# Kernel tuning notes

Measured on AMD Instinct MI355X. Metric: run time of the kernel, lower is better.

Reference implementation:

```python
import jax, jax.numpy as jnp
import numpy as np

N, E, IN, H, O, K = 50000, 800000, 256, 128, 32, 5
ALPHA, EPS = 0.1, 1e-5


def setup_inputs() -> dict:
    key = jax.random.key(0)
    ks = jax.random.split(key, 20)
    nrm = lambda k, shape, s=0.02: jax.random.normal(k, shape, dtype=jnp.float32) * s
    H2 = H // 2
    return {
        "x": jax.random.normal(ks[0], (N, IN), dtype=jnp.float32),
        "edge_index": jax.random.randint(ks[1], (2, E), 0, N),
        "edge_weight": jax.random.uniform(ks[2], (E,), dtype=jnp.float32),
        # lin1 + bn1
        "W1": nrm(ks[3], (IN, H)), "b1": jnp.zeros((H,), jnp.float32),
        "g1": jnp.ones((H,), jnp.float32), "be1": jnp.zeros((H,), jnp.float32),
        "m1": nrm(ks[4], (H,), 0.1), "v1": 1.0 + 0.1 * jax.random.uniform(ks[5], (H,), dtype=jnp.float32),
        # lin2 + bn2
        "W2": nrm(ks[6], (H, H)), "b2": jnp.zeros((H,), jnp.float32),
        "g2": jnp.ones((H,), jnp.float32), "be2": jnp.zeros((H,), jnp.float32),
        "m2": nrm(ks[7], (H,), 0.1), "v2": 1.0 + 0.1 * jax.random.uniform(ks[8], (H,), dtype=jnp.float32),
        # attention over hop outputs (K+1)
        "att": jnp.ones((K + 1,), jnp.float32) + nrm(ks[9], (K + 1,), 0.1),
        # head: Linear(H, H//2) + BN + ReLU + Linear(H//2, O)
        "W3": nrm(ks[10], (H, H2)), "b3": jnp.zeros((H2,), jnp.float32),
        "g3": jnp.ones((H2,), jnp.float32), "be3": jnp.zeros((H2,), jnp.float32),
        "m3": nrm(ks[11], (H2,), 0.1), "v3": 1.0 + 0.1 * jax.random.uniform(ks[12], (H2,), dtype=jnp.float32),
        "W4": nrm(ks[13], (H2, O)), "b4": jnp.zeros((O,), jnp.float32),
    }


def _bn(t, g, b, m, v):
    # eval-mode BatchNorm1d using running stats
    return (t - m) * (g / jnp.sqrt(v + EPS)) + b


def reference(x, edge_index, edge_weight, W1, b1, g1, be1, m1, v1,
              W2, b2, g2, be2, m2, v2, att,
              W3, b3, g3, be3, m3, v3, W4, b4):
    n = x.shape[0]
    row, col = edge_index[0], edge_index[1]

    h = jax.nn.relu(_bn(x @ W1 + b1, g1, be1, m1, v1))
    identity = h
    h = jax.nn.relu(_bn(h @ W2 + b2, g2, be2, m2, v2)) + identity

    # weighted edge normalization: out-weight sum per source node, clamped >= 1
    wsum = jnp.maximum(jax.ops.segment_sum(edge_weight, row, num_segments=n), 1.0)
    edge_norm = edge_weight / wsum[row]  # [E]

    def prop(h_in):
        # APPNP-style: K inner iterations blending toward this call's h0
        h0 = h_in
        hk = h_in
        for _ in range(K):
            msg = hk[row] * edge_norm[:, None]          # [E, H] gather + scale
            agg = jax.ops.segment_sum(msg, col, num_segments=n)  # scatter-add
            hk = (1.0 - ALPHA) * agg + ALPHA * h0
        return hk

    xs = [h]
    hc = h
    for _ in range(K):  # outer loop: att has K+1 weights
        hc = prop(hc)
        xs.append(hc)

    stacked = jnp.stack(xs, axis=-1)          # [N, H, K+1]
    w = jax.nn.softmax(att)                   # [K+1]
    fused = jnp.einsum('nhk,k->nh', stacked, w)

    hid = jax.nn.relu(_bn(fused @ W3 + b3, g3, be3, m3, v3))
    return hid @ W4 + b4
```

## Files before the change

kernel.cpp:

```cpp
#include <hip/hip_runtime.h>
#include <cstddef>
#include <cstdint>

namespace {

constexpr int N   = 50000;
constexpr int E   = 800000;
constexpr int IN  = 256;
constexpr int H   = 128;
constexpr int H2v = 64;
constexpr int O   = 32;
constexpr int K   = 5;
constexpr float ALPHA = 0.1f;
constexpr float EPS   = 1e-5f;
constexpr int SCAN_CH = 1024;
constexpr int SCAN_NB = (N + SCAN_CH - 1) / SCAN_CH;

__device__ inline uint32_t pack2_bf16(float x, float y) {
  uint32_t ux = __float_as_uint(x);
  uint32_t uy = __float_as_uint(y);
  ux = (ux + 0x7FFFu + ((ux >> 16) & 1u)) >> 16;
  uy = (uy + 0x7FFFu + ((uy >> 16) & 1u)) & 0xFFFF0000u;
  return uy | ux;
}

__device__ inline float bf16_lo(uint32_t v) { return __uint_as_float(v << 16); }
__device__ inline float bf16_hi(uint32_t v) { return __uint_as_float(v & 0xFFFF0000u); }

__global__ void zero_int_kernel(int* __restrict__ p, int n) {
  int i = blockIdx.x * blockDim.x + threadIdx.x;
  if (i < n) p[i] = 0;
}

__global__ void softmax_att_kernel(const float* __restrict__ att, float* __restrict__ wk) {
  if (threadIdx.x == 0 && blockIdx.x == 0) {
    float mx = att[0];
    for (int i = 1; i < K + 1; ++i) mx = fmaxf(mx, att[i]);
    float ex[K + 1];
    float s = 0.f;
    for (int i = 0; i < K + 1; ++i) { ex[i] = expf(att[i] - mx); s += ex[i]; }
    for (int i = 0; i < K + 1; ++i) wk[i] = ex[i] / s;
  }
}

__global__ void hist_kernel(const int* __restrict__ row, const int* __restrict__ col,
                            const float* __restrict__ ew,
                            int* __restrict__ deg, float* __restrict__ wsum) {
  int i = blockIdx.x * blockDim.x + threadIdx.x;
  if (i < E) {
    atomicAdd(&deg[col[i]], 1);
    atomicAdd(&wsum[row[i]], ew[i]);
  }
}

__global__ __launch_bounds__(256) void scan_local_kernel(const int* __restrict__ deg,
                                                         int* __restrict__ offs,
                                                         int* __restrict__ bsum) {
  __shared__ int sd[256];
  int base = blockIdx.x * SCAN_CH;
  int t = threadIdx.x;
  int v[4];
  int s = 0;
#pragma unroll
  for (int u = 0; u < 4; ++u) {
    int i = base + t * 4 + u;
    v[u] = (i < N) ? deg[i] : 0;
    s += v[u];
  }
  sd[t] = s;
  __syncthreads();
  int val = s;
  for (int off = 1; off < 256; off <<= 1) {
    int x = (t >= off) ? sd[t - off] : 0;
    __syncthreads();
    val += x;
    sd[t] = val;
    __syncthreads();
  }
  int excl = val - s;
#pragma unroll
  for (int u = 0; u < 4; ++u) {
    int i = base + t * 4 + u;
    if (i < N) offs[i] = excl;
    excl += v[u];
  }
  if (t == 255) bsum[blockIdx.x] = val;
}

__global__ void scan_bsum_kernel(int* __restrict__ bsum) {
  if (threadIdx.x == 0 && blockIdx.x == 0) {
    int acc = 0;
    for (int i = 0; i < SCAN_NB; ++i) {
      int v = bsum[i];
      bsum[i] = acc;
      acc += v;
    }
    bsum[SCAN_NB] = acc;
  }
}

__global__ void scan_add_kernel(int* __restrict__ offs, const int* __restrict__ bsum,
                                int* __restrict__ cursor) {
  int i = blockIdx.x * blockDim.x + threadIdx.x;
  if (i < N) {
    int o = offs[i] + bsum[i / SCAN_CH];
    offs[i] = o;
    cursor[i] = o;
  }
  if (i == 0) offs[N] = bsum[SCAN_NB];
}

__global__ void fill_kernel(const int* __restrict__ row, const int* __restrict__ col,
                            const float* __restrict__ ew, const float* __restrict__ wsum,
                            int* __restrict__ cursor, int* __restrict__ csr_src,
                            float* __restrict__ csr_w) {
  int i = blockIdx.x * blockDim.x + threadIdx.x;
  if (i < E) {
    int d = col[i];
    int p = atomicAdd(&cursor[d], 1);
    int s = row[i];
    csr_src[p] = s;
    csr_w[p] = ew[i] / fmaxf(wsum[s], 1.0f);
  }
}

__global__ __launch_bounds__(256) void mlp1_kernel(
    const float* __restrict__ x, const float* __restrict__ W1,
    const float* __restrict__ b1, const float* __restrict__ g1,
    const float* __restrict__ be1, const float* __restrict__ m1,
    const float* __restrict__ v1, float* __restrict__ h1) {
  __shared__ float xl[32][IN];
  int node0 = blockIdx.x * 32;
  int t = threadIdx.x;
  for (int idx = t * 4; idx < 32 * IN; idx += 256 * 4) {
    int r = idx >> 8, c = idx & (IN - 1);
    float4 xv = {0.f, 0.f, 0.f, 0.f};
    if (node0 + r < N) xv = *(const float4*)&x[(size_t)(node0 + r) * IN + c];
    *(float4*)&xl[r][c] = xv;
  }
  __syncthreads();
  int ng = t >> 5;
  int c0 = (t & 31) * 4;
  float acc[4][4];
#pragma unroll
  for (int a = 0; a < 4; ++a)
#pragma unroll
    for (int b = 0; b < 4; ++b) acc[a][b] = 0.f;
  for (int k = 0; k < IN; k += 4) {
    float4 xv[4];
#pragma unroll
    for (int a = 0; a < 4; ++a) xv[a] = *(const float4*)&xl[ng * 4 + a][k];
    float4 wv[4];
#pragma unroll
    for (int j = 0; j < 4; ++j) wv[j] = *(const float4*)&W1[(size_t)(k + j) * H + c0];
#pragma unroll
    for (int a = 0; a < 4; ++a) {
      float xa0 = xv[a].x, xa1 = xv[a].y, xa2 = xv[a].z, xa3 = xv[a].w;
      acc[a][0] += xa0 * wv[0].x + xa1 * wv[1].x + xa2 * wv[2].x + xa3 * wv[3].x;
      acc[a][1] += xa0 * wv[0].y + xa1 * wv[1].y + xa2 * wv[2].y + xa3 * wv[3].y;
      acc[a][2] += xa0 * wv[0].z + xa1 * wv[1].z + xa2 * wv[2].z + xa3 * wv[3].z;
      acc[a][3] += xa0 * wv[0].w + xa1 * wv[1].w + xa2 * wv[2].w + xa3 * wv[3].w;
    }
  }
  float sc[4], ad[4], bb[4];
#pragma unroll
  for (int b = 0; b < 4; ++b) {
    int c = c0 + b;
    sc[b] = g1[c] * rsqrtf(v1[c] + EPS);
    ad[b] = b1[c] - m1[c];
    bb[b] = be1[c];
  }
#pragma unroll
  for (int a = 0; a < 4; ++a) {
    int node = node0 + ng * 4 + a;
    if (node < N) {
      float4 o;
      o.x = fmaxf((acc[a][0] + ad[0]) * sc[0] + bb[0], 0.f);
      o.y = fmaxf((acc[a][1] + ad[1]) * sc[1] + bb[1], 0.f);
      o.z = fmaxf((acc[a][2] + ad[2]) * sc[2] + bb[2], 0.f);
      o.w = fmaxf((acc[a][3] + ad[3]) * sc[3] + bb[3], 0.f);
      *(float4*)&h1[(size_t)node * H + c0] = o;
    }
  }
}

__global__ __launch_bounds__(128) void mlp2_kernel(
    const float* __restrict__ h1, const float* __restrict__ W2,
    const float* __restrict__ b2, const float* __restrict__ g2,
    const float* __restrict__ be2, const float* __restrict__ m2,
    const float* __restrict__ v2, unsigned short* __restrict__ h0bf,
    float* __restrict__ fused, const float* __restrict__ wk) {
  __shared__ float xl[16][H];
  int node0 = blockIdx.x * 16;
  int t = threadIdx.x;
  for (int idx = t * 4; idx < 16 * H; idx += 128 * 4) {
    int r = idx >> 7, c = idx & (H - 1);
    *(float4*)&xl[r][c] = *(const float4*)&h1[(size_t)(node0 + r) * H + c];
  }
  __syncthreads();
  int ng = t >> 5;
  int c0 = (t & 31) * 4;
  float acc[4][4];
#pragma unroll
  for (int a = 0; a < 4; ++a)
#pragma unroll
    for (int b = 0; b < 4; ++b) acc[a][b] = 0.f;
  for (int k = 0; k < H; k += 4) {
    float4 xv[4];
#pragma unroll
    for (int a = 0; a < 4; ++a) xv[a] = *(const float4*)&xl[ng * 4 + a][k];
    float4 wv[4];
#pragma unroll
    for (int j = 0; j < 4; ++j) wv[j] = *(const float4*)&W2[(size_t)(k + j) * H + c0];
#pragma unroll
    for (int a = 0; a < 4; ++a) {
      float xa0 = xv[a].x, xa1 = xv[a].y, xa2 = xv[a].z, xa3 = xv[a].w;
      acc[a][0] += xa0 * wv[0].x + xa1 * wv[1].x + xa2 * wv[2].x + xa3 * wv[3].x;
      acc[a][1] += xa0 * wv[0].y + xa1 * wv[1].y + xa2 * wv[2].y + xa3 * wv[3].y;
      acc[a][2] += xa0 * wv[0].z + xa1 * wv[1].z + xa2 * wv[2].z + xa3 * wv[3].z;
      acc[a][3] += xa0 * wv[0].w + xa1 * wv[1].w + xa2 * wv[2].w + xa3 * wv[3].w;
    }
  }
  float sc[4], ad[4], bb[4];
#pragma unroll
  for (int b = 0; b < 4; ++b) {
    int c = c0 + b;
    sc[b] = g2[c] * rsqrtf(v2[c] + EPS);
    ad[b] = b2[c] - m2[c];
    bb[b] = be2[c];
  }
  float w0 = wk[0];
#pragma unroll
  for (int a = 0; a < 4; ++a) {
    int node = node0 + ng * 4 + a;
    float r0 = fmaxf((acc[a][0] + ad[0]) * sc[0] + bb[0], 0.f) + xl[ng * 4 + a][c0 + 0];
    float r1 = fmaxf((acc[a][1] + ad[1]) * sc[1] + bb[1], 0.f) + xl[ng * 4 + a][c0 + 1];
    float r2 = fmaxf((acc[a][2] + ad[2]) * sc[2] + bb[2], 0.f) + xl[ng * 4 + a][c0 + 2];
    float r3 = fmaxf((acc[a][3] + ad[3]) * sc[3] + bb[3], 0.f) + xl[ng * 4 + a][c0 + 3];
    uint2 pk;
    pk.x = pack2_bf16(r0, r1);
    pk.y = pack2_bf16(r2, r3);
    *(uint2*)&h0bf[(size_t)node * H + c0] = pk;
    float4 f = {w0 * r0, w0 * r1, w0 * r2, w0 * r3};
    *(float4*)&fused[(size_t)node * H + c0] = f;
  }
}

__global__ __launch_bounds__(256) void prop_kernel(
    const unsigned short* __restrict__ hk, const unsigned short* __restrict__ h0,
    unsigned short* __restrict__ outb,
    const int* __restrict__ offs, const int* __restrict__ csr_src,
    const float* __restrict__ csr_w,
    float* __restrict__ fused, const float* __restrict__ wk, int wj) {
  int wave = threadIdx.x >> 6;
  int lane = threadIdx.x & 63;
  int node = blockIdx.x * 4 + wave;
  if (node >= N) return;
  int beg = offs[node];
  int end = offs[node + 1];
  int c = lane * 2;
  float ax = 0.f, ay = 0.f;
  int e = beg;
  for (; e + 8 <= end; e += 8) {
    int s[8];
    float w[8];
    uint32_t v[8];
#pragma unroll
    for (int u = 0; u < 8; ++u) { s[u] = csr_src[e + u]; w[u] = csr_w[e + u]; }
#pragma unroll
    for (int u = 0; u < 8; ++u) { v[u] = *(const uint32_t*)&hk[(size_t)s[u] * H + c]; }
#pragma unroll
    for (int u = 0; u < 8; ++u) {
      ax += w[u] * bf16_lo(v[u]);
      ay += w[u] * bf16_hi(v[u]);
    }
  }
  for (; e < end; ++e) {
    int s = csr_src[e];
    float w = csr_w[e];
    uint32_t v = *(const uint32_t*)&hk[(size_t)s * H + c];
    ax += w * bf16_lo(v);
    ay += w * bf16_hi(v);
  }
  size_t idx = (size_t)node * H + c;
  uint32_t hv = *(const uint32_t*)&h0[idx];
  float vx = (1.f - ALPHA) * ax + ALPHA * bf16_lo(hv);
  float vy = (1.f - ALPHA) * ay + ALPHA * bf16_hi(hv);
  *(uint32_t*)&outb[idx] = pack2_bf16(vx, vy);
  if (wj >= 0) {
    float w = wk[wj];
    float2 f = *(float2*)&fused[idx];
    f.x += w * vx;
    f.y += w * vy;
    *(float2*)&fused[idx] = f;
  }
}

__global__ __launch_bounds__(64) void head_kernel(
    const float* __restrict__ fused, const float* __restrict__ W3,
    const float* __restrict__ b3, const float* __restrict__ g3,
    const float* __restrict__ be3, const float* __restrict__ m3,
    const float* __restrict__ v3, const float* __restrict__ W4,
    const float* __restrict__ b4, float* __restrict__ out) {
  __shared__ float fl[16][H];
  __shared__ float hl[16][H2v];
  int node0 = blockIdx.x * 16;
  int t = threadIdx.x;
  for (int idx = t * 4; idx < 16 * H; idx += 64 * 4) {
    int r = idx >> 7, c = idx & (H - 1);
    *(float4*)&fl[r][c] = *(const float4*)&fused[(size_t)(node0 + r) * H + c];
  }
  __syncthreads();
  {
    int ng = t >> 4;
    int c0 = (t & 15) * 4;
    float acc[4][4];
#pragma unroll
    for (int a = 0; a < 4; ++a)
#pragma unroll
      for (int b = 0; b < 4; ++b) acc[a][b] = 0.f;
    for (int k = 0; k < H; k += 4) {
      float4 xv[4];
#pragma unroll
      for (int a = 0; a < 4; ++a) xv[a] = *(const float4*)&fl[ng * 4 + a][k];
      float4 wv[4];
#pragma unroll
      for (int j = 0; j < 4; ++j) wv[j] = *(const float4*)&W3[(size_t)(k + j) * H2v + c0];
#pragma unroll
      for (int a = 0; a < 4; ++a) {
        float xa0 = xv[a].x, xa1 = xv[a].y, xa2 = xv[a].z, xa3 = xv[a].w;
        acc[a][0] += xa0 * wv[0].x + xa1 * wv[1].x + xa2 * wv[2].x + xa3 * wv[3].x;
        acc[a][1] += xa0 * wv[0].y + xa1 * wv[1].y + xa2 * wv[2].y + xa3 * wv[3].y;
        acc[a][2] += xa0 * wv[0].z + xa1 * wv[1].z + xa2 * wv[2].z + xa3 * wv[3].z;
        acc[a][3] += xa0 * wv[0].w + xa1 * wv[1].w + xa2 * wv[2].w + xa3 * wv[3].w;
      }
    }
    float sc[4], ad[4], bb[4];
#pragma unroll
    for (int b = 0; b < 4; ++b) {
      int c = c0 + b;
      sc[b] = g3[c] * rsqrtf(v3[c] + EPS);
      ad[b] = b3[c] - m3[c];
      bb[b] = be3[c];
    }
#pragma unroll
    for (int a = 0; a < 4; ++a) {
#pragma unroll
      for (int b = 0; b < 4; ++b) {
        hl[ng * 4 + a][c0 + b] = fmaxf((acc[a][b] + ad[b]) * sc[b] + bb[b], 0.f);
      }
    }
  }
  __syncthreads();
  {
    int co = t & 31;
    int nh = t >> 5;
    float bias = b4[co];
#pragma unroll
    for (int a = 0; a < 8; ++a) {
      int nloc = nh * 8 + a;
      float accf = bias;
      for (int k = 0; k < H2v; k += 4) {
        float4 hv = *(const float4*)&hl[nloc][k];
        accf += hv.x * W4[(size_t)(k + 0) * O + co];
        accf += hv.y * W4[(size_t)(k + 1) * O + co];
        accf += hv.z * W4[(size_t)(k + 2) * O + co];
        accf += hv.w * W4[(size_t)(k + 3) * O + co];
      }
      out[(size_t)(node0 + nloc) * O + co] = accf;
    }
  }
}

}

extern "C" void kernel_launch(void* const* d_in, const int* in_sizes, int n_in,
                              void* d_out, int out_size, void* d_ws, size_t ws_size,
                              hipStream_t stream) {
  const float* x   = (const float*)d_in[0];
  const int*   ei  = (const int*)d_in[1];
  const float* ew  = (const float*)d_in[2];
  const float* W1  = (const float*)d_in[3];
  const float* b1  = (const float*)d_in[4];
  const float* g1  = (const float*)d_in[5];
  const float* be1 = (const float*)d_in[6];
  const float* m1  = (const float*)d_in[7];
  const float* v1  = (const float*)d_in[8];
  const float* W2  = (const float*)d_in[9];
  const float* b2  = (const float*)d_in[10];
  const float* g2  = (const float*)d_in[11];
  const float* be2 = (const float*)d_in[12];
  const float* m2  = (const float*)d_in[13];
  const float* v2  = (const float*)d_in[14];
  const float* att = (const float*)d_in[15];
  const float* W3  = (const float*)d_in[16];
  const float* b3  = (const float*)d_in[17];
  const float* g3  = (const float*)d_in[18];
  const float* be3 = (const float*)d_in[19];
  const float* m3  = (const float*)d_in[20];
  const float* v3  = (const float*)d_in[21];
  const float* W4  = (const float*)d_in[22];
  const float* b4  = (const float*)d_in[23];
  const int* row = ei;
  const int* col = ei + E;
  float* out = (float*)d_out;

  char* p = (char*)d_ws;
  auto carve = [&](size_t bytes) -> void* {
    void* q = (void*)p;
    p += (bytes + 255) & ~(size_t)255;
    return q;
  };
  int*   deg     = (int*)carve((size_t)N * 4);
  float* wsum    = (float*)carve((size_t)N * 4);
  int*   offs    = (int*)carve((size_t)(N + 1) * 4);
  int*   cursor  = (int*)carve((size_t)N * 4);
  int*   bsum    = (int*)carve((size_t)(SCAN_NB + 1) * 4);
  int*   csr_src = (int*)carve((size_t)E * 4);
  float* csr_w   = (float*)carve((size_t)E * 4);
  float* wk      = (float*)carve(64);
  float* h1      = (float*)carve((size_t)N * H * 4);
  unsigned short* bf0 = (unsigned short*)carve((size_t)N * H * 2);
  unsigned short* bfA = (unsigned short*)carve((size_t)N * H * 2);
  unsigned short* bfB = (unsigned short*)carve((size_t)N * H * 2);
  float* fused   = (float*)carve((size_t)N * H * 4);

  const int tb = 256;
  zero_int_kernel<<<(N + tb - 1) / tb, tb, 0, stream>>>(deg, N);
  zero_int_kernel<<<(N + tb - 1) / tb, tb, 0, stream>>>((int*)wsum, N);
  softmax_att_kernel<<<1, 64, 0, stream>>>(att, wk);
  hist_kernel<<<(E + tb - 1) / tb, tb, 0, stream>>>(row, col, ew, deg, wsum);
  scan_local_kernel<<<SCAN_NB, 256, 0, stream>>>(deg, offs, bsum);
  scan_bsum_kernel<<<1, 64, 0, stream>>>(bsum);
  scan_add_kernel<<<(N + tb - 1) / tb, tb, 0, stream>>>(offs, bsum, cursor);
  fill_kernel<<<(E + tb - 1) / tb, tb, 0, stream>>>(row, col, ew, wsum, cursor, csr_src, csr_w);

  mlp1_kernel<<<(N + 31) / 32, 256, 0, stream>>>(x, W1, b1, g1, be1, m1, v1, h1);
  mlp2_kernel<<<(N + 15) / 16, 128, 0, stream>>>(h1, W2, b2, g2, be2, m2, v2, bf0, fused, wk);

  unsigned short* h0 = bf0;
  unsigned short* pa = bfA;
  unsigned short* pb = bfB;
  for (int j = 1; j <= K; ++j) {
    const unsigned short* src = h0;
    unsigned short* dst = pa;
    for (int i = 0; i < K; ++i) {
      int wj = (i == K - 1) ? j : -1;
      prop_kernel<<<(N + 3) / 4, 256, 0, stream>>>(src, h0, dst, offs, csr_src, csr_w, fused, wk, wj);
      if (i < K - 1) {
        src = dst;
        dst = (dst == pa) ? pb : pa;
      }
    }
    unsigned short* oldh0 = h0;
    h0 = pa;
    pa = pb;
    pb = oldh0;
  }

  head_kernel<<<(N + 15) / 16, 64, 0, stream>>>(fused, W3, b3, g3, be3, m3, v3, W4, b4, out);
}
```

Before: 1.420 ms.

## Use bf16 MFMA for MLP layers, interleave CSR, multi-node prop waves

Replaces the FP32 SIMT MLP1/MLP2 kernels with bf16 MFMA 16x16x32 kernels. This requires per-call conversion of x and the transposed weights to bf16 and padding to a multiple of 64 rows. It also packs the CSR source index and weight into one uint2 array, so each edge needs a single load. Each prop wave now handles 8 nodes instead of one, with an extra 4-wide unrolled tail, and the two zero kernels are merged. The conversions add an extra pass over x, and bf16 inputs to the first matmul reduce precision.

```diff
diff --git a/kernel.cpp b/kernel.cpp
--- a/kernel.cpp
+++ b/kernel.cpp
@@ -15,6 +15,11 @@
 constexpr float EPS   = 1e-5f;
 constexpr int SCAN_CH = 1024;
 constexpr int SCAN_NB = (N + SCAN_CH - 1) / SCAN_CH;
+constexpr int NPAD = 50048;
+constexpr int NPW  = 8;
+
+typedef __bf16 bf16x8 __attribute__((ext_vector_type(8)));
+typedef float  f32x4  __attribute__((ext_vector_type(4)));
 
 __device__ inline uint32_t pack2_bf16(float x, float y) {
   uint32_t ux = __float_as_uint(x);
@@ -23,13 +28,17 @@
   uy = (uy + 0x7FFFu + ((uy >> 16) & 1u)) & 0xFFFF0000u;
   return uy | ux;
 }
-
+__device__ inline unsigned short bf16_1(float x) {
+  uint32_t u = __float_as_uint(x);
+  return (unsigned short)((u + 0x7FFFu + ((u >> 16) & 1u)) >> 16);
+}
 __device__ inline float bf16_lo(uint32_t v) { return __uint_as_float(v << 16); }
 __device__ inline float bf16_hi(uint32_t v) { return __uint_as_float(v & 0xFFFF0000u); }
-
-__global__ void zero_int_kernel(int* __restrict__ p, int n) {
+__device__ inline float bf16_f(unsigned short h) { return __uint_as_float(((uint32_t)h) << 16); }
+
+__global__ void zero2_kernel(int* __restrict__ a, int* __restrict__ b, int n) {
   int i = blockIdx.x * blockDim.x + threadIdx.x;
-  if (i < n) p[i] = 0;
+  if (i < n) { a[i] = 0; b[i] = 0; }
 }
 
 __global__ void softmax_att_kernel(const float* __restrict__ att, float* __restrict__ wk) {
@@ -112,187 +121,192 @@
 
 __global__ void fill_kernel(const int* __restrict__ row, const int* __restrict__ col,
                             const float* __restrict__ ew, const float* __restrict__ wsum,
-                            int* __restrict__ cursor, int* __restrict__ csr_src,
-                            float* __restrict__ csr_w) {
+                            int* __restrict__ cursor, uint2* __restrict__ csr) {
   int i = blockIdx.x * blockDim.x + threadIdx.x;
   if (i < E) {
     int d = col[i];
     int p = atomicAdd(&cursor[d], 1);
     int s = row[i];
-    csr_src[p] = s;
-    csr_w[p] = ew[i] / fmaxf(wsum[s], 1.0f);
-  }
-}
-
-__global__ __launch_bounds__(256) void mlp1_kernel(
-    const float* __restrict__ x, const float* __restrict__ W1,
+    float w = ew[i] / fmaxf(wsum[s], 1.0f);
+    csr[p] = make_uint2((uint32_t)s, __float_as_uint(w));
+  }
+}
+
+__global__ void conv_x_kernel(const float* __restrict__ x, unsigned short* __restrict__ xbf) {
+  int i = blockIdx.x * blockDim.x + threadIdx.x;
+  size_t base = (size_t)i * 8;
+  int r = (int)(base / IN);
+  uint4 pk = {0, 0, 0, 0};
+  if (r < N) {
+    float4 a = *(const float4*)&x[base];
+    float4 b = *(const float4*)&x[base + 4];
+    pk.x = pack2_bf16(a.x, a.y);
+    pk.y = pack2_bf16(a.z, a.w);
+    pk.z = pack2_bf16(b.x, b.y);
+    pk.w = pack2_bf16(b.z, b.w);
+  }
+  *(uint4*)&xbf[base] = pk;
+}
+
+__global__ void conv_wt_kernel(const float* __restrict__ W, unsigned short* __restrict__ Wt,
+                               int Kdim) {
+  int t = blockIdx.x * blockDim.x + threadIdx.x;
+  int k8 = Kdim / 8;
+  int n = t / k8;
+  int kk = (t % k8) * 8;
+  if (n >= H) return;
+  float f[8];
+#pragma unroll
+  for (int j = 0; j < 8; ++j) f[j] = W[(size_t)(kk + j) * H + n];
+  uint4 pk;
+  pk.x = pack2_bf16(f[0], f[1]);
+  pk.y = pack2_bf16(f[2], f[3]);
+  pk.z = pack2_bf16(f[4], f[5]);
+  pk.w = pack2_bf16(f[6], f[7]);
+  *(uint4*)&Wt[(size_t)n * Kdim + kk] = pk;
+}
+
+__global__ __launch_bounds__(256) void mlp1_mfma_kernel(
+    const unsigned short* __restrict__ xbf, const unsigned short* __restrict__ Wt1,
     const float* __restrict__ b1, const float* __restrict__ g1,
     const float* __restrict__ be1, const float* __restrict__ m1,
-    const float* __restrict__ v1, float* __restrict__ h1) {
-  __shared__ float xl[32][IN];
-  int node0 = blockIdx.x * 32;
-  int t = threadIdx.x;
-  for (int idx = t * 4; idx < 32 * IN; idx += 256 * 4) {
-    int r = idx >> 8, c = idx & (IN - 1);
-    float4 xv = {0.f, 0.f, 0.f, 0.f};
-    if (node0 + r < N) xv = *(const float4*)&x[(size_t)(node0 + r) * IN + c];
-    *(float4*)&xl[r][c] = xv;
-  }
-  __syncthreads();
-  int ng = t >> 5;
-  int c0 = (t & 31) * 4;
-  float acc[4][4];
-#pragma unroll
-  for (int a = 0; a < 4; ++a)
-#pragma unroll
-    for (int b = 0; b < 4; ++b) acc[a][b] = 0.f;
-  for (int k = 0; k < IN; k += 4) {
-    float4 xv[4];
-#pragma unroll
-    for (int a = 0; a < 4; ++a) xv[a] = *(const float4*)&xl[ng * 4 + a][k];
-    float4 wv[4];
-#pragma unroll
-    for (int j = 0; j < 4; ++j) wv[j] = *(const float4*)&W1[(size_t)(k + j) * H + c0];
-#pragma unroll
-    for (int a = 0; a < 4; ++a) {
-      float xa0 = xv[a].x, xa1 = xv[a].y, xa2 = xv[a].z, xa3 = xv[a].w;
-      acc[a][0] += xa0 * wv[0].x + xa1 * wv[1].x + xa2 * wv[2].x + xa3 * wv[3].x;
-      acc[a][1] += xa0 * wv[0].y + xa1 * wv[1].y + xa2 * wv[2].y + xa3 * wv[3].y;
-      acc[a][2] += xa0 * wv[0].z + xa1 * wv[1].z + xa2 * wv[2].z + xa3 * wv[3].z;
-      acc[a][3] += xa0 * wv[0].w + xa1 * wv[1].w + xa2 * wv[2].w + xa3 * wv[3].w;
-    }
-  }
-  float sc[4], ad[4], bb[4];
-#pragma unroll
-  for (int b = 0; b < 4; ++b) {
-    int c = c0 + b;
-    sc[b] = g1[c] * rsqrtf(v1[c] + EPS);
-    ad[b] = b1[c] - m1[c];
-    bb[b] = be1[c];
-  }
-#pragma unroll
-  for (int a = 0; a < 4; ++a) {
-    int node = node0 + ng * 4 + a;
-    if (node < N) {
-      float4 o;
-      o.x = fmaxf((acc[a][0] + ad[0]) * sc[0] + bb[0], 0.f);
-      o.y = fmaxf((acc[a][1] + ad[1]) * sc[1] + bb[1], 0.f);
-      o.z = fmaxf((acc[a][2] + ad[2]) * sc[2] + bb[2], 0.f);
-      o.w = fmaxf((acc[a][3] + ad[3]) * sc[3] + bb[3], 0.f);
-      *(float4*)&h1[(size_t)node * H + c0] = o;
-    }
-  }
-}
-
-__global__ __launch_bounds__(128) void mlp2_kernel(
-    const float* __restrict__ h1, const float* __restrict__ W2,
+    const float* __restrict__ v1, unsigned short* __restrict__ h1bf) {
+  int wave = threadIdx.x >> 6;
+  int lane = threadIdx.x & 63;
+  int m_base = blockIdx.x * 64 + wave * 16;
+  int idx16 = lane & 15;
+  int quad = lane >> 4;
+  bf16x8 afrag[8];
+  const unsigned short* xrow = xbf + (size_t)(m_base + idx16) * IN + quad * 8;
+#pragma unroll
+  for (int k0 = 0; k0 < 8; ++k0) afrag[k0] = *(const bf16x8*)(xrow + k0 * 32);
+#pragma unroll
+  for (int n0 = 0; n0 < 8; ++n0) {
+    f32x4 acc = {0.f, 0.f, 0.f, 0.f};
+    const unsigned short* wrow = Wt1 + (size_t)(n0 * 16 + idx16) * IN + quad * 8;
+#pragma unroll
+    for (int k0 = 0; k0 < 8; ++k0) {
+      bf16x8 bfrag = *(const bf16x8*)(wrow + k0 * 32);
+      acc = __builtin_amdgcn_mfma_f32_16x16x32_bf16(afrag[k0], bfrag, acc, 0, 0, 0);
+    }
+    int n = n0 * 16 + idx16;
+    float sc = g1[n] * rsqrtf(v1[n] + EPS);
+    float ad = b1[n] - m1[n];
+    float bb = be1[n];
+#pragma unroll
+    for (int r = 0; r < 4; ++r) {
+      int m = m_base + quad * 4 + r;
+      float val = fmaxf((acc[r] + ad) * sc + bb, 0.f);
+      h1bf[(size_t)m * H + n] = bf16_1(val);
+    }
+  }
+}
+
+__global__ __launch_bounds__(256) void mlp2_mfma_kernel(
+    const unsigned short* __restrict__ h1bf, const unsigned short* __restrict__ Wt2,
     const float* __restrict__ b2, const float* __restrict__ g2,
     const float* __restrict__ be2, const float* __restrict__ m2,
     const float* __restrict__ v2, unsigned short* __restrict__ h0bf,
     float* __restrict__ fused, const float* __restrict__ wk) {
-  __shared__ float xl[16][H];
-  int node0 = blockIdx.x * 16;
-  int t = threadIdx.x;
-  for (int idx = t * 4; idx < 16 * H; idx += 128 * 4) {
-    int r = idx >> 7, c = idx & (H - 1);
-    *(float4*)&xl[r][c] = *(const float4*)&h1[(size_t)(node0 + r) * H + c];
-  }
-  __syncthreads();
-  int ng = t >> 5;
-  int c0 = (t & 31) * 4;
-  float acc[4][4];
-#pragma unroll
-  for (int a = 0; a < 4; ++a)
-#pragma unroll
-    for (int b = 0; b < 4; ++b) acc[a][b] = 0.f;
-  for (int k = 0; k < H; k += 4) {
-    float4 xv[4];
-#pragma unroll
-    for (int a = 0; a < 4; ++a) xv[a] = *(const float4*)&xl[ng * 4 + a][k];
-    float4 wv[4];
-#pragma unroll
-    for (int j = 0; j < 4; ++j) wv[j] = *(const float4*)&W2[(size_t)(k + j) * H + c0];
-#pragma unroll
-    for (int a = 0; a < 4; ++a) {
-      float xa0 = xv[a].x, xa1 = xv[a].y, xa2 = xv[a].z, xa3 = xv[a].w;
-      acc[a][0] += xa0 * wv[0].x + xa1 * wv[1].x + xa2 * wv[2].x + xa3 * wv[3].x;
-      acc[a][1] += xa0 * wv[0].y + xa1 * wv[1].y + xa2 * wv[2].y + xa3 * wv[3].y;
-      acc[a][2] += xa0 * wv[0].z + xa1 * wv[1].z + xa2 * wv[2].z + xa3 * wv[3].z;
-      acc[a][3] += xa0 * wv[0].w + xa1 * wv[1].w + xa2 * wv[2].w + xa3 * wv[3].w;
-    }
-  }
-  float sc[4], ad[4], bb[4];
-#pragma unroll
-  for (int b = 0; b < 4; ++b) {
-    int c = c0 + b;
-    sc[b] = g2[c] * rsqrtf(v2[c] + EPS);
-    ad[b] = b2[c] - m2[c];
-    bb[b] = be2[c];
-  }
+  int wave = threadIdx.x >> 6;
+  int lane = threadIdx.x & 63;
+  int m_base = blockIdx.x * 64 + wave * 16;
+  int idx16 = lane & 15;
+  int quad = lane >> 4;
+  bf16x8 afrag[4];
+  const unsigned short* arow = h1bf + (size_t)(m_base + idx16) * H + quad * 8;
+#pragma unroll
+  for (int k0 = 0; k0 < 4; ++k0) afrag[k0] = *(const bf16x8*)(arow + k0 * 32);
   float w0 = wk[0];
 #pragma unroll
-  for (int a = 0; a < 4; ++a) {
-    int node = node0 + ng * 4 + a;
-    float r0 = fmaxf((acc[a][0] + ad[0]) * sc[0] + bb[0], 0.f) + xl[ng * 4 + a][c0 + 0];
-    float r1 = fmaxf((acc[a][1] + ad[1]) * sc[1] + bb[1], 0.f) + xl[ng * 4 + a][c0 + 1];
-    float r2 = fmaxf((acc[a][2] + ad[2]) * sc[2] + bb[2], 0.f) + xl[ng * 4 + a][c0 + 2];
-    float r3 = fmaxf((acc[a][3] + ad[3]) * sc[3] + bb[3], 0.f) + xl[ng * 4 + a][c0 + 3];
-    uint2 pk;
-    pk.x = pack2_bf16(r0, r1);
-    pk.y = pack2_bf16(r2, r3);
-    *(uint2*)&h0bf[(size_t)node * H + c0] = pk;
-    float4 f = {w0 * r0, w0 * r1, w0 * r2, w0 * r3};
-    *(float4*)&fused[(size_t)node * H + c0] = f;
+  for (int n0 = 0; n0 < 8; ++n0) {
+    f32x4 acc = {0.f, 0.f, 0.f, 0.f};
+    const unsigned short* wrow = Wt2 + (size_t)(n0 * 16 + idx16) * H + quad * 8;
+#pragma unroll
+    for (int k0 = 0; k0 < 4; ++k0) {
+      bf16x8 bfrag = *(const bf16x8*)(wrow + k0 * 32);
+      acc = __builtin_amdgcn_mfma_f32_16x16x32_bf16(afrag[k0], bfrag, acc, 0, 0, 0);
+    }
+    int n = n0 * 16 + idx16;
+    float sc = g2[n] * rsqrtf(v2[n] + EPS);
+    float ad = b2[n] - m2[n];
+    float bb = be2[n];
+#pragma unroll
+    for (int r = 0; r < 4; ++r) {
+      int m = m_base + quad * 4 + r;
+      if (m < N) {
+        float idv = bf16_f(h1bf[(size_t)m * H + n]);
+        float val = fmaxf((acc[r] + ad) * sc + bb, 0.f) + idv;
+        h0bf[(size_t)m * H + n] = bf16_1(val);
+        fused[(size_t)m * H + n] = w0 * val;
+      }
+    }
   }
 }
 
 __global__ __launch_bounds__(256) void prop_kernel(
     const unsigned short* __restrict__ hk, const unsigned short* __restrict__ h0,
     unsigned short* __restrict__ outb,
-    const int* __restrict__ offs, const int* __restrict__ csr_src,
-    const float* __restrict__ csr_w,
+    const int* __restrict__ offs, const uint2* __restrict__ csr,
     float* __restrict__ fused, const float* __restrict__ wk, int wj) {
   int wave = threadIdx.x >> 6;
   int lane = threadIdx.x & 63;
-  int node = blockIdx.x * 4 + wave;
-  if (node >= N) return;
-  int beg = offs[node];
-  int end = offs[node + 1];
+  int node0 = (blockIdx.x * 4 + wave) * NPW;
   int c = lane * 2;
-  float ax = 0.f, ay = 0.f;
-  int e = beg;
-  for (; e + 8 <= end; e += 8) {
-    int s[8];
-    float w[8];
-    uint32_t v[8];
-#pragma unroll
-    for (int u = 0; u < 8; ++u) { s[u] = csr_src[e + u]; w[u] = csr_w[e + u]; }
-#pragma unroll
-    for (int u = 0; u < 8; ++u) { v[u] = *(const uint32_t*)&hk[(size_t)s[u] * H + c]; }
-#pragma unroll
-    for (int u = 0; u < 8; ++u) {
-      ax += w[u] * bf16_lo(v[u]);
-      ay += w[u] * bf16_hi(v[u]);
-    }
-  }
-  for (; e < end; ++e) {
-    int s = csr_src[e];
-    float w = csr_w[e];
-    uint32_t v = *(const uint32_t*)&hk[(size_t)s * H + c];
-    ax += w * bf16_lo(v);
-    ay += w * bf16_hi(v);
-  }
-  size_t idx = (size_t)node * H + c;
-  uint32_t hv = *(const uint32_t*)&h0[idx];
-  float vx = (1.f - ALPHA) * ax + ALPHA * bf16_lo(hv);
-  float vy = (1.f - ALPHA) * ay + ALPHA * bf16_hi(hv);
-  *(uint32_t*)&outb[idx] = pack2_bf16(vx, vy);
-  if (wj >= 0) {
-    float w = wk[wj];
-    float2 f = *(float2*)&fused[idx];
-    f.x += w * vx;
-    f.y += w * vy;
-    *(float2*)&fused[idx] = f;
+  float wj_w = (wj >= 0) ? wk[wj] : 0.f;
+  for (int nn = 0; nn < NPW; ++nn) {
+    int node = node0 + nn;
+    if (node >= N) return;
+    int beg = offs[node];
+    int end = offs[node + 1];
+    float ax = 0.f, ay = 0.f;
+    int e = beg;
+    for (; e + 8 <= end; e += 8) {
+      uint2 ew[8];
+#pragma unroll
+      for (int u = 0; u < 8; ++u) ew[u] = csr[e + u];
+      uint32_t v[8];
+#pragma unroll
+      for (int u = 0; u < 8; ++u) v[u] = *(const uint32_t*)&hk[(size_t)ew[u].x * H + c];
+#pragma unroll
+      for (int u = 0; u < 8; ++u) {
+        float w = __uint_as_float(ew[u].y);
+        ax += w * bf16_lo(v[u]);
+        ay += w * bf16_hi(v[u]);
+      }
+    }
+    for (; e + 4 <= end; e += 4) {
+      uint2 ew[4];
+#pragma unroll
+      for (int u = 0; u < 4; ++u) ew[u] = csr[e + u];
+      uint32_t v[4];
+#pragma unroll
+      for (int u = 0; u < 4; ++u) v[u] = *(const uint32_t*)&hk[(size_t)ew[u].x * H + c];
+#pragma unroll
+      for (int u = 0; u < 4; ++u) {
+        float w = __uint_as_float(ew[u].y);
+        ax += w * bf16_lo(v[u]);
+        ay += w * bf16_hi(v[u]);
+      }
+    }
+    for (; e < end; ++e) {
+      uint2 ew = csr[e];
+      float w = __uint_as_float(ew.y);
+      uint32_t v = *(const uint32_t*)&hk[(size_t)ew.x * H + c];
+      ax += w * bf16_lo(v);
+      ay += w * bf16_hi(v);
+    }
+    size_t idx = (size_t)node * H + c;
+    uint32_t hv = *(const uint32_t*)&h0[idx];
+    float vx = (1.f - ALPHA) * ax + ALPHA * bf16_lo(hv);
+    float vy = (1.f - ALPHA) * ay + ALPHA * bf16_hi(hv);
+    *(uint32_t*)&outb[idx] = pack2_bf16(vx, vy);
+    if (wj >= 0) {
+      float2 f = *(float2*)&fused[idx];
+      f.x += wj_w * vx;
+      f.y += wj_w * vy;
+      *(float2*)&fused[idx] = f;
+    }
   }
 }
 
@@ -344,12 +358,10 @@
       bb[b] = be3[c];
     }
 #pragma unroll
-    for (int a = 0; a < 4; ++a) {
-#pragma unroll
-      for (int b = 0; b < 4; ++b) {
+    for (int a = 0; a < 4; ++a)
+#pragma unroll
+      for (int b = 0; b < 4; ++b)
         hl[ng * 4 + a][c0 + b] = fmaxf((acc[a][b] + ad[b]) * sc[b] + bb[b], 0.f);
-      }
-    }
   }
   __syncthreads();
   {
@@ -416,37 +428,44 @@
   int*   offs    = (int*)carve((size_t)(N + 1) * 4);
   int*   cursor  = (int*)carve((size_t)N * 4);
   int*   bsum    = (int*)carve((size_t)(SCAN_NB + 1) * 4);
-  int*   csr_src = (int*)carve((size_t)E * 4);
-  float* csr_w   = (float*)carve((size_t)E * 4);
+  uint2* csr     = (uint2*)carve((size_t)E * 8);
   float* wk      = (float*)carve(64);
-  float* h1      = (float*)carve((size_t)N * H * 4);
-  unsigned short* bf0 = (unsigned short*)carve((size_t)N * H * 2);
-  unsigned short* bfA = (unsigned short*)carve((size_t)N * H * 2);
-  unsigned short* bfB = (unsigned short*)carve((size_t)N * H * 2);
+  unsigned short* xbf  = (unsigned short*)carve((size_t)NPAD * IN * 2);
+  unsigned short* Wt1  = (unsigned short*)carve((size_t)H * IN * 2);
+  unsigned short* Wt2  = (unsigned short*)carve((size_t)H * H * 2);
+  unsigned short* h1bf = (unsigned short*)carve((size_t)NPAD * H * 2);
+  unsigned short* bf0  = (unsigned short*)carve((size_t)N * H * 2);
+  unsigned short* bfA  = (unsigned short*)carve((size_t)N * H * 2);
+  unsigned short* bfB  = (unsigned short*)carve((size_t)N * H * 2);
   float* fused   = (float*)carve((size_t)N * H * 4);
 
   const int tb = 256;
-  zero_int_kernel<<<(N + tb - 1) / tb, tb, 0, stream>>>(deg, N);
-  zero_int_kernel<<<(N + tb - 1) / tb, tb, 0, stream>>>((int*)wsum, N);
+  zero2_kernel<<<(N + tb - 1) / tb, tb, 0, stream>>>(deg, (int*)wsum, N);
   softmax_att_kernel<<<1, 64, 0, stream>>>(att, wk);
   hist_kernel<<<(E + tb - 1) / tb, tb, 0, stream>>>(row, col, ew, deg, wsum);
   scan_local_kernel<<<SCAN_NB, 256, 0, stream>>>(deg, offs, bsum);
   scan_bsum_kernel<<<1, 64, 0, stream>>>(bsum);
   scan_add_kernel<<<(N + tb - 1) / tb, tb, 0, stream>>>(offs, bsum, cursor);
-  fill_kernel<<<(E + tb - 1) / tb, tb, 0, stream>>>(row, col, ew, wsum, cursor, csr_src, csr_w);
-
-  mlp1_kernel<<<(N + 31) / 32, 256, 0, stream>>>(x, W1, b1, g1, be1, m1, v1, h1);
-  mlp2_kernel<<<(N + 15) / 16, 128, 0, stream>>>(h1, W2, b2, g2, be2, m2, v2, bf0, fused, wk);
+  fill_kernel<<<(E + tb - 1) / tb, tb, 0, stream>>>(row, col, ew, wsum, cursor, csr);
+
+  conv_x_kernel<<<(NPAD * IN / 8 + tb - 1) / tb, tb, 0, stream>>>(x, xbf);
+  conv_wt_kernel<<<(H * (IN / 8) + tb - 1) / tb, tb, 0, stream>>>(W1, Wt1, IN);
+  conv_wt_kernel<<<(H * (H / 8) + tb - 1) / tb, tb, 0, stream>>>(W2, Wt2, H);
+
+  mlp1_mfma_kernel<<<NPAD / 64, 256, 0, stream>>>(xbf, Wt1, b1, g1, be1, m1, v1, h1bf);
+  mlp2_mfma_kernel<<<NPAD / 64, 256, 0, stream>>>(h1bf, Wt2, b2, g2, be2, m2, v2,
+                                                  bf0, fused, wk);
 
   unsigned short* h0 = bf0;
   unsigned short* pa = bfA;
   unsigned short* pb = bfB;
+  const int prop_blocks = (N + 4 * NPW - 1) / (4 * NPW);
   for (int j = 1; j <= K; ++j) {
     const unsigned short* src = h0;
     unsigned short* dst = pa;
     for (int i = 0; i < K; ++i) {
       int wj = (i == K - 1) ? j : -1;
-      prop_kernel<<<(N + 3) / 4, 256, 0, stream>>>(src, h0, dst, offs, csr_src, csr_w, fused, wk, wj);
+      prop_kernel<<<prop_blocks, 256, 0, stream>>>(src, h0, dst, offs, csr, fused, wk, wj);
       if (i < K - 1) {
         src = dst;
         dst = (dst == pa) ? pb : pa;
@@ -458,5 +477,5 @@
     pb = oldh0;
   }
 
-  head_kernel<<<(N + 15) / 16, 64, 0, stream>>>(fused, W3, b3, g3, be3, m3, v3, W4, b4, out);
-}
+  head_kernel<<<N / 16, 64, 0, stream>>>(fused, W3, b3, g3, be3, m3, v3, W4, b4, out);
+}
```

New measurement: 1.323 ms. 6.9% less time.
